# Kernel optimization log

Measured on AMD Instinct MI355X. Metric: run time of the kernel, lower is better.

The kernel has to match this reference:

```python
import jax, jax.numpy as jnp
import numpy as np

VOCAB = 32000
HIDDEN = 512
B, T = 8, 512
LN_EPS = 1e-5


def setup_inputs() -> dict:
    key = jax.random.key(0)
    ks = jax.random.split(key, 9)
    s = 0.02
    return {
        "input_ids": jax.random.randint(ks[0], (B, T), 0, VOCAB),
        "emb": jax.random.normal(ks[1], (VOCAB, HIDDEN), jnp.float32) * s,
        "w_ih": jax.random.normal(ks[2], (3 * HIDDEN, HIDDEN), jnp.float32) * s,
        "w_hh": jax.random.normal(ks[3], (3 * HIDDEN, HIDDEN), jnp.float32) * s,
        "b_ih": jnp.zeros((3 * HIDDEN,), jnp.float32),
        "b_hh": jnp.zeros((3 * HIDDEN,), jnp.float32),
        "ln_gamma": jnp.ones((HIDDEN,), jnp.float32),
        "ln_beta": jnp.zeros((HIDDEN,), jnp.float32),
        "head_w": jax.random.normal(ks[4], (VOCAB, HIDDEN), jnp.float32) * s,
        "head_b": jnp.zeros((VOCAB,), jnp.float32),
    }


def _gru_scan(xg, w_hh, b_hh):
    # xg: [T, B, 3H]  (input-side gate pre-activations, PyTorch gate order r,z,n)
    H = xg.shape[-1] // 3
    h0 = jnp.zeros((xg.shape[1], H), xg.dtype)

    def step(h, xg_t):
        hg = h @ w_hh.T + b_hh              # [B, 3H]
        xr, xz, xn = jnp.split(xg_t, 3, axis=-1)
        hr, hz, hn = jnp.split(hg, 3, axis=-1)
        r = jax.nn.sigmoid(xr + hr)
        z = jax.nn.sigmoid(xz + hz)
        n = jnp.tanh(xn + r * hn)
        h_new = (1.0 - z) * n + z * h
        return h_new, h_new

    _, hs = jax.lax.scan(step, h0, xg)
    return hs  # [T, B, H]


def reference(input_ids, emb, w_ih, w_hh, b_ih, b_hh, ln_gamma, ln_beta, head_w, head_b):
    # embedding lookup: [B, T, H]
    x = emb[input_ids]
    # precompute input-side gate pre-activations for all timesteps: [B, T, 3H]
    xg = jnp.einsum("bth,gh->btg", x, w_ih) + b_ih
    # sequential GRU over time
    hs = _gru_scan(jnp.swapaxes(xg, 0, 1), w_hh, b_hh)  # [T, B, H]
    hs = jnp.swapaxes(hs, 0, 1)                          # [B, T, H]
    # LayerNorm over hidden dim
    mu = jnp.mean(hs, axis=-1, keepdims=True)
    var = jnp.mean(jnp.square(hs - mu), axis=-1, keepdims=True)
    y = (hs - mu) * jax.lax.rsqrt(var + LN_EPS) * ln_gamma + ln_beta
    # output head: [B, T, V]
    logits = jnp.einsum("bth,vh->btv", y, head_w) + head_b
    return logits
```

## Files before the change

kernel.cpp:

```cpp
#include <hip/hip_runtime.h>
#include <hip/hip_bf16.h>
#include <stdint.h>

#define VOCAB 32000
#define HID 512
#define NB 8
#define SEQ 512
#define NG 1536
#define LN_EPS 1e-5f
#define GRU_WGS 32
#define GRU_SPIN_BUDGET (1 << 20)

typedef short bf16x8 __attribute__((ext_vector_type(8)));
typedef float f32x4 __attribute__((ext_vector_type(4)));

__device__ __forceinline__ unsigned short f2bf(float f) {
  union { float f; uint32_t u; } c; c.f = f;
  return (unsigned short)((c.u + 0x7fffu + ((c.u >> 16) & 1u)) >> 16);
}

__global__ void init_ws_kernel(unsigned short* h_state, int* flags) {
  int i = blockIdx.x * 256 + threadIdx.x;
  if (i < 2 * 16 * HID) h_state[i] = 0;
  if (i < GRU_WGS * 16) flags[i] = 0;
}

__global__ void conv_bf16_kernel(const float* __restrict__ in,
                                 unsigned short* __restrict__ out, int n4) {
  int i = blockIdx.x * 256 + threadIdx.x;
  if (i >= n4) return;
  const float4 v = ((const float4*)in)[i];
  ushort4 o;
  o.x = f2bf(v.x); o.y = f2bf(v.y); o.z = f2bf(v.z); o.w = f2bf(v.w);
  ((ushort4*)out)[i] = o;
}

__global__ void embed_kernel(const int* __restrict__ ids,
                             const float* __restrict__ emb,
                             unsigned short* __restrict__ out) {
  int row = blockIdx.x;
  int id = ids[row];
  int c = threadIdx.x * 2;
  const float2 v = *(const float2*)(emb + (size_t)id * HID + c);
  ushort2 o; o.x = f2bf(v.x); o.y = f2bf(v.y);
  *(ushort2*)(out + (size_t)row * HID + c) = o;
}

#define BM 128
#define BN 128
#define BK 32

__global__ __launch_bounds__(256, 2) void gemm_bt_kernel(
    const unsigned short* __restrict__ A, const unsigned short* __restrict__ B,
    const float* __restrict__ bias, float* __restrict__ C, int N, int nbn) {
  __shared__ unsigned short a_lds[BM * BK];
  __shared__ unsigned short b_lds[BN * BK];
  const int nwg = gridDim.x;
  const int chunk = nwg >> 3;
  const int bid = blockIdx.x;
  const int sw = (bid & 7) * chunk + (bid >> 3);
  const int bm = sw / nbn, bn = sw % nbn;
  const int tid = threadIdx.x;
  const int lane = tid & 63, wid = tid >> 6;
  const int wm = wid >> 1, wn = wid & 1;

  f32x4 acc[4][4] = {};

  for (int kt = 0; kt < HID / BK; ++kt) {
    __syncthreads();
#pragma unroll
    for (int p = 0; p < 2; ++p) {
      const int flat = (p * 256 + tid) * 16;
      const int row = flat >> 6;
      const int kb = flat & 63;
      const char* ga =
          (const char*)(A + ((size_t)(bm * BM + row) * HID + kt * BK)) + kb;
      const char* gb =
          (const char*)(B + ((size_t)(bn * BN + row) * HID + kt * BK)) + kb;
      char* la = (char*)a_lds + (size_t)(p * 256 + wid * 64) * 16;
      char* lb = (char*)b_lds + (size_t)(p * 256 + wid * 64) * 16;
      __builtin_amdgcn_global_load_lds(
          (const __attribute__((address_space(1))) void*)ga,
          (__attribute__((address_space(3))) void*)la, 16, 0, 0);
      __builtin_amdgcn_global_load_lds(
          (const __attribute__((address_space(1))) void*)gb,
          (__attribute__((address_space(3))) void*)lb, 16, 0, 0);
    }
    __syncthreads();
    bf16x8 af[4], bfr[4];
#pragma unroll
    for (int i = 0; i < 4; ++i) {
      af[i] = *(const bf16x8*)(a_lds + (wm * 64 + i * 16 + (lane & 15)) * BK +
                               (lane >> 4) * 8);
      bfr[i] = *(const bf16x8*)(b_lds + (wn * 64 + i * 16 + (lane & 15)) * BK +
                                (lane >> 4) * 8);
    }
#pragma unroll
    for (int i = 0; i < 4; ++i)
#pragma unroll
      for (int j = 0; j < 4; ++j)
        acc[i][j] =
            __builtin_amdgcn_mfma_f32_16x16x32_bf16(af[i], bfr[j], acc[i][j], 0, 0, 0);
  }
#pragma unroll
  for (int i = 0; i < 4; ++i) {
    const int mrow = bm * BM + wm * 64 + i * 16 + (lane >> 4) * 4;
#pragma unroll
    for (int j = 0; j < 4; ++j) {
      const int col = bn * BN + wn * 64 + j * 16 + (lane & 15);
      const float bv = bias[col];
#pragma unroll
      for (int r = 0; r < 4; ++r)
        C[(size_t)(mrow + r) * N + col] = acc[i][j][r] + bv;
    }
  }
}

__global__ __launch_bounds__(192, 1) void gru_kernel(
    const float* __restrict__ xg, const float* __restrict__ w_hh,
    const float* __restrict__ b_hh, float* __restrict__ hs,
    unsigned short* h_state, int* flags) {
  const int wid = blockIdx.x;
  const int tid = threadIdx.x;
  const int lane = tid & 63;
  const int g = tid >> 6;

  __shared__ float hg_lds[3 * 128];
  __shared__ float bhh_lds[48];

  bf16x8 wf[16];
  {
    const int row = g * HID + wid * 16 + (lane & 15);
    const float* wr = w_hh + (size_t)row * HID + (lane >> 4) * 8;
#pragma unroll
    for (int kk = 0; kk < 16; ++kk) {
      float4 f0 = *(const float4*)(wr + kk * 32);
      float4 f1 = *(const float4*)(wr + kk * 32 + 4);
      bf16x8 v;
      v[0] = (short)f2bf(f0.x); v[1] = (short)f2bf(f0.y);
      v[2] = (short)f2bf(f0.z); v[3] = (short)f2bf(f0.w);
      v[4] = (short)f2bf(f1.x); v[5] = (short)f2bf(f1.y);
      v[6] = (short)f2bf(f1.z); v[7] = (short)f2bf(f1.w);
      wf[kk] = v;
    }
  }
  if (tid < 48) bhh_lds[tid] = b_hh[(tid >> 4) * HID + wid * 16 + (tid & 15)];
  __syncthreads();

  const int abase = (lane & 15) * HID + (lane >> 4) * 8;
  const bool realrow = (lane & 15) < 8;
  const int myflag = (lane & 31) * 16;
  const int b8 = tid >> 4, n16 = tid & 15;
  const size_t xoff0 = (size_t)b8 * SEQ * NG + wid * 16 + n16;

  float xr = 0.f, xz = 0.f, xn = 0.f;
  if (tid < 128) {
    xr = xg[xoff0];
    xz = xg[xoff0 + HID];
    xn = xg[xoff0 + 2 * HID];
  }
  float hprev = 0.f;
  int budget = GRU_SPIN_BUDGET;

  for (int t = 0; t < SEQ; ++t) {
    const unsigned short* rd = h_state + (size_t)(t & 1) * (16 * HID);
    unsigned short* wr_ = h_state + (size_t)((t + 1) & 1) * (16 * HID);

    uint64_t hb[32];
#pragma unroll
    for (int kk = 0; kk < 32; ++kk) hb[kk] = 0;
    if (realrow) {
#pragma unroll
      for (int kk = 0; kk < 16; ++kk) {
        const uint64_t* ap = (const uint64_t*)(rd + abase + kk * 32);
        hb[2 * kk] =
            __hip_atomic_load(ap, __ATOMIC_RELAXED, __HIP_MEMORY_SCOPE_AGENT);
        hb[2 * kk + 1] = __hip_atomic_load(ap + 1, __ATOMIC_RELAXED,
                                           __HIP_MEMORY_SCOPE_AGENT);
      }
    }
    f32x4 acc = {0.f, 0.f, 0.f, 0.f};
#pragma unroll
    for (int kk = 0; kk < 16; ++kk) {
      union { uint64_t u[2]; bf16x8 v; } cv;
      cv.u[0] = hb[2 * kk]; cv.u[1] = hb[2 * kk + 1];
      acc = __builtin_amdgcn_mfma_f32_16x16x32_bf16(cv.v, wf[kk], acc, 0, 0, 0);
    }
    if (lane < 32) {
      const int m0 = (lane >> 4) * 4;
#pragma unroll
      for (int r = 0; r < 4; ++r)
        hg_lds[g * 128 + (m0 + r) * 16 + (lane & 15)] = acc[r];
    }
    __syncthreads();
    if (tid < 128) {
      const float hrv = hg_lds[tid] + bhh_lds[n16];
      const float hzv = hg_lds[128 + tid] + bhh_lds[16 + n16];
      const float hnv = hg_lds[256 + tid] + bhh_lds[32 + n16];
      const float r = 1.f / (1.f + __expf(-(xr + hrv)));
      const float z = 1.f / (1.f + __expf(-(xz + hzv)));
      const float a = xn + r * hnv;
      const float e2 = __expf(-2.f * fabsf(a));
      const float nn = copysignf((1.f - e2) / (1.f + e2), a);
      const float hnew = (1.f - z) * nn + z * hprev;
      hprev = hnew;
      hs[((size_t)b8 * SEQ + t) * HID + wid * 16 + n16] = hnew;
      const float hnb = __shfl_down(hnew, 1);
      if ((n16 & 1) == 0) {
        union { unsigned short s[2]; uint32_t u; } pk;
        pk.s[0] = f2bf(hnew); pk.s[1] = f2bf(hnb);
        uint32_t* dst = (uint32_t*)(wr_ + b8 * HID + wid * 16 + n16);
        __hip_atomic_store(dst, pk.u, __ATOMIC_RELAXED,
                           __HIP_MEMORY_SCOPE_AGENT);
      }
    }
    __syncthreads();
    if (tid == 0)
      __hip_atomic_store(flags + wid * 16, t + 1, __ATOMIC_RELAXED,
                         __HIP_MEMORY_SCOPE_AGENT);
    if (tid < 128 && t + 1 < SEQ) {
      const size_t xo = xoff0 + (size_t)(t + 1) * NG;
      xr = xg[xo]; xz = xg[xo + HID]; xn = xg[xo + 2 * HID];
    }
    if (tid < 64) {
      while (budget > 0) {
        int v = __hip_atomic_load(flags + myflag, __ATOMIC_RELAXED,
                                  __HIP_MEMORY_SCOPE_AGENT);
        if (__ballot(v >= t + 1) == ~0ULL) break;
        --budget;
        __builtin_amdgcn_s_sleep(1);
      }
    }
    __syncthreads();
  }
}

__global__ __launch_bounds__(256) void ln_kernel(
    const float* __restrict__ hs, const float* __restrict__ gamma,
    const float* __restrict__ beta, unsigned short* __restrict__ y) {
  const int row = blockIdx.x * 4 + (threadIdx.x >> 6);
  const int lane = threadIdx.x & 63;
  const float* x = hs + (size_t)row * HID + lane * 8;
  float v[8];
  *(float4*)v = *(const float4*)x;
  *(float4*)(v + 4) = *(const float4*)(x + 4);
  float s = 0.f, q = 0.f;
#pragma unroll
  for (int j = 0; j < 8; ++j) { s += v[j]; q += v[j] * v[j]; }
#pragma unroll
  for (int off = 32; off > 0; off >>= 1) {
    s += __shfl_xor(s, off);
    q += __shfl_xor(q, off);
  }
  const float mu = s * (1.f / 512.f);
  const float is = rsqrtf(q * (1.f / 512.f) - mu * mu + LN_EPS);
  const float* gp = gamma + lane * 8;
  const float* bp = beta + lane * 8;
  union { unsigned short o[8]; uint4 u; } pk;
#pragma unroll
  for (int j = 0; j < 8; ++j) pk.o[j] = f2bf((v[j] - mu) * is * gp[j] + bp[j]);
  *(uint4*)(y + (size_t)row * HID + lane * 8) = pk.u;
}

extern "C" void kernel_launch(void* const* d_in, const int* in_sizes, int n_in,
                              void* d_out, int out_size, void* d_ws,
                              size_t ws_size, hipStream_t stream) {
  const int* ids = (const int*)d_in[0];
  const float* emb = (const float*)d_in[1];
  const float* w_ih = (const float*)d_in[2];
  const float* w_hh = (const float*)d_in[3];
  const float* b_ih = (const float*)d_in[4];
  const float* b_hh = (const float*)d_in[5];
  const float* gamma = (const float*)d_in[6];
  const float* beta = (const float*)d_in[7];
  const float* head_w = (const float*)d_in[8];
  const float* head_b = (const float*)d_in[9];
  float* out = (float*)d_out;

  char* ws = (char*)d_ws;
  size_t off = 0;
  auto alloc = [&](size_t bytes) -> void* {
    void* p = ws + off;
    off = (off + bytes + 255) & ~(size_t)255;
    return p;
  };
  int* flags = (int*)alloc(GRU_WGS * 16 * sizeof(int));
  unsigned short* h_state = (unsigned short*)alloc(2 * 16 * HID * 2);
  unsigned short* A1 = (unsigned short*)alloc((size_t)NB * SEQ * HID * 2);
  unsigned short* wihb = (unsigned short*)alloc((size_t)NG * HID * 2);
  unsigned short* hwb = (unsigned short*)alloc((size_t)VOCAB * HID * 2);
  float* xg = (float*)alloc((size_t)NB * SEQ * NG * 4);
  float* hsb = (float*)alloc((size_t)NB * SEQ * HID * 4);
  unsigned short* yb = (unsigned short*)alloc((size_t)NB * SEQ * HID * 2);

  init_ws_kernel<<<64, 256, 0, stream>>>(h_state, flags);
  conv_bf16_kernel<<<(NG * HID / 4) / 256, 256, 0, stream>>>(w_ih, wihb,
                                                             NG * HID / 4);
  conv_bf16_kernel<<<(VOCAB * HID / 4) / 256, 256, 0, stream>>>(
      head_w, hwb, VOCAB * HID / 4);
  embed_kernel<<<NB * SEQ, 256, 0, stream>>>(ids, emb, A1);
  gemm_bt_kernel<<<(NB * SEQ / BM) * (NG / BN), 256, 0, stream>>>(
      A1, wihb, b_ih, xg, NG, NG / BN);
  gru_kernel<<<GRU_WGS, 192, 0, stream>>>(xg, w_hh, b_hh, hsb, h_state, flags);
  ln_kernel<<<NB * SEQ / 4, 256, 0, stream>>>(hsb, gamma, beta, yb);
  gemm_bt_kernel<<<(NB * SEQ / BM) * (VOCAB / BN), 256, 0, stream>>>(
      yb, hwb, head_b, out, VOCAB, VOCAB / BN);
}
```

Before: 1.980 ms.

## Replace GRU flag barrier with parity bits embedded in published hidden state

Drops the separate per-workgroup flag array and spin-wait barrier in the persistent GRU kernel. The low mantissa bit of every other bf16 hidden value now carries a step-parity tag, and consumers re-poll only the stale 64-bit chunks until every tag matches. This removes one store, one barrier and a flag round trip per timestep. It costs one bit of hidden-state precision and relies on the ordering of the relaxed atomic stores. The MFMA chain is also split into two accumulators for more instruction-level parallelism.

New measurement: 2.418 ms. 22.2% more time.

```diff
diff --git a/kernel.cpp b/kernel.cpp
--- a/kernel.cpp
+++ b/kernel.cpp
@@ -19,10 +19,10 @@
   return (unsigned short)((c.u + 0x7fffu + ((c.u >> 16) & 1u)) >> 16);
 }
 
-__global__ void init_ws_kernel(unsigned short* h_state, int* flags) {
+__global__ void init_ws_kernel(unsigned short* h_state) {
   int i = blockIdx.x * 256 + threadIdx.x;
-  if (i < 2 * 16 * HID) h_state[i] = 0;
-  if (i < GRU_WGS * 16) flags[i] = 0;
+  if (i < 16 * HID) h_state[i] = 0;
+  else if (i < 2 * 16 * HID) h_state[i] = 1;
 }
 
 __global__ void conv_bf16_kernel(const float* __restrict__ in,
@@ -119,7 +119,7 @@
 __global__ __launch_bounds__(192, 1) void gru_kernel(
     const float* __restrict__ xg, const float* __restrict__ w_hh,
     const float* __restrict__ b_hh, float* __restrict__ hs,
-    unsigned short* h_state, int* flags) {
+    unsigned short* h_state) {
   const int wid = blockIdx.x;
   const int tid = threadIdx.x;
   const int lane = tid & 63;
@@ -149,7 +149,6 @@
 
   const int abase = (lane & 15) * HID + (lane >> 4) * 8;
   const bool realrow = (lane & 15) < 8;
-  const int myflag = (lane & 31) * 16;
   const int b8 = tid >> 4, n16 = tid & 15;
   const size_t xoff0 = (size_t)b8 * SEQ * NG + wid * 16 + n16;
 
@@ -164,28 +163,44 @@
 
   for (int t = 0; t < SEQ; ++t) {
     const unsigned short* rd = h_state + (size_t)(t & 1) * (16 * HID);
-    unsigned short* wr_ = h_state + (size_t)((t + 1) & 1) * (16 * HID);
+    unsigned short* wpub = h_state + (size_t)((t + 1) & 1) * (16 * HID);
+    const uint32_t texp = (uint32_t)((t >> 1) & 1);
+    const uint32_t tpub = (uint32_t)(((t + 1) >> 1) & 1);
 
     uint64_t hb[32];
 #pragma unroll
     for (int kk = 0; kk < 32; ++kk) hb[kk] = 0;
-    if (realrow) {
+    uint32_t stale = realrow ? 0xFFFFFFFFu : 0u;
+    while (stale) {
 #pragma unroll
       for (int kk = 0; kk < 16; ++kk) {
         const uint64_t* ap = (const uint64_t*)(rd + abase + kk * 32);
-        hb[2 * kk] =
-            __hip_atomic_load(ap, __ATOMIC_RELAXED, __HIP_MEMORY_SCOPE_AGENT);
-        hb[2 * kk + 1] = __hip_atomic_load(ap + 1, __ATOMIC_RELAXED,
-                                           __HIP_MEMORY_SCOPE_AGENT);
+        if (stale & (1u << (2 * kk)))
+          hb[2 * kk] = __hip_atomic_load(ap, __ATOMIC_RELAXED,
+                                         __HIP_MEMORY_SCOPE_AGENT);
+        if (stale & (1u << (2 * kk + 1)))
+          hb[2 * kk + 1] = __hip_atomic_load(ap + 1, __ATOMIC_RELAXED,
+                                             __HIP_MEMORY_SCOPE_AGENT);
       }
-    }
-    f32x4 acc = {0.f, 0.f, 0.f, 0.f};
-#pragma unroll
-    for (int kk = 0; kk < 16; ++kk) {
-      union { uint64_t u[2]; bf16x8 v; } cv;
-      cv.u[0] = hb[2 * kk]; cv.u[1] = hb[2 * kk + 1];
-      acc = __builtin_amdgcn_mfma_f32_16x16x32_bf16(cv.v, wf[kk], acc, 0, 0, 0);
-    }
+#pragma unroll
+      for (int kk = 0; kk < 32; ++kk) {
+        const uint32_t lo = (uint32_t)hb[kk];
+        const uint32_t hi = (uint32_t)(hb[kk] >> 32);
+        if ((((lo ^ texp) | (hi ^ texp)) & 1u) == 0u) stale &= ~(1u << kk);
+      }
+      if (--budget <= 0) break;
+    }
+
+    f32x4 acc0 = {0.f, 0.f, 0.f, 0.f}, acc1 = {0.f, 0.f, 0.f, 0.f};
+#pragma unroll
+    for (int kk = 0; kk < 16; kk += 2) {
+      union { uint64_t u[2]; bf16x8 v; } c0, c1;
+      c0.u[0] = hb[2 * kk];     c0.u[1] = hb[2 * kk + 1];
+      c1.u[0] = hb[2 * kk + 2]; c1.u[1] = hb[2 * kk + 3];
+      acc0 = __builtin_amdgcn_mfma_f32_16x16x32_bf16(c0.v, wf[kk], acc0, 0, 0, 0);
+      acc1 = __builtin_amdgcn_mfma_f32_16x16x32_bf16(c1.v, wf[kk + 1], acc1, 0, 0, 0);
+    }
+    const f32x4 acc = acc0 + acc1;
     if (lane < 32) {
       const int m0 = (lane >> 4) * 4;
 #pragma unroll
@@ -208,28 +223,16 @@
       const float hnb = __shfl_down(hnew, 1);
       if ((n16 & 1) == 0) {
         union { unsigned short s[2]; uint32_t u; } pk;
-        pk.s[0] = f2bf(hnew); pk.s[1] = f2bf(hnb);
-        uint32_t* dst = (uint32_t*)(wr_ + b8 * HID + wid * 16 + n16);
+        pk.s[0] = (unsigned short)((f2bf(hnew) & ~(unsigned short)1) | tpub);
+        pk.s[1] = f2bf(hnb);
+        uint32_t* dst = (uint32_t*)(wpub + b8 * HID + wid * 16 + n16);
         __hip_atomic_store(dst, pk.u, __ATOMIC_RELAXED,
                            __HIP_MEMORY_SCOPE_AGENT);
       }
     }
-    __syncthreads();
-    if (tid == 0)
-      __hip_atomic_store(flags + wid * 16, t + 1, __ATOMIC_RELAXED,
-                         __HIP_MEMORY_SCOPE_AGENT);
     if (tid < 128 && t + 1 < SEQ) {
       const size_t xo = xoff0 + (size_t)(t + 1) * NG;
       xr = xg[xo]; xz = xg[xo + HID]; xn = xg[xo + 2 * HID];
-    }
-    if (tid < 64) {
-      while (budget > 0) {
-        int v = __hip_atomic_load(flags + myflag, __ATOMIC_RELAXED,
-                                  __HIP_MEMORY_SCOPE_AGENT);
-        if (__ballot(v >= t + 1) == ~0ULL) break;
-        --budget;
-        __builtin_amdgcn_s_sleep(1);
-      }
     }
     __syncthreads();
   }
@@ -284,7 +287,6 @@
     off = (off + bytes + 255) & ~(size_t)255;
     return p;
   };
-  int* flags = (int*)alloc(GRU_WGS * 16 * sizeof(int));
   unsigned short* h_state = (unsigned short*)alloc(2 * 16 * HID * 2);
   unsigned short* A1 = (unsigned short*)alloc((size_t)NB * SEQ * HID * 2);
   unsigned short* wihb = (unsigned short*)alloc((size_t)NG * HID * 2);
@@ -293,7 +295,7 @@
   float* hsb = (float*)alloc((size_t)NB * SEQ * HID * 4);
   unsigned short* yb = (unsigned short*)alloc((size_t)NB * SEQ * HID * 2);
 
-  init_ws_kernel<<<64, 256, 0, stream>>>(h_state, flags);
+  init_ws_kernel<<<64, 256, 0, stream>>>(h_state);
   conv_bf16_kernel<<<(NG * HID / 4) / 256, 256, 0, stream>>>(w_ih, wihb,
                                                              NG * HID / 4);
   conv_bf16_kernel<<<(VOCAB * HID / 4) / 256, 256, 0, stream>>>(
@@ -301,7 +303,7 @@
   embed_kernel<<<NB * SEQ, 256, 0, stream>>>(ids, emb, A1);
   gemm_bt_kernel<<<(NB * SEQ / BM) * (NG / BN), 256, 0, stream>>>(
       A1, wihb, b_ih, xg, NG, NG / BN);
-  gru_kernel<<<GRU_WGS, 192, 0, stream>>>(xg, w_hh, b_hh, hsb, h_state, flags);
+  gru_kernel<<<GRU_WGS, 192, 0, stream>>>(xg, w_hh, b_hh, hsb, h_state);
   ln_kernel<<<NB * SEQ / 4, 256, 0, stream>>>(hsb, gamma, beta, yb);
   gemm_bt_kernel<<<(NB * SEQ / BM) * (VOCAB / BN), 256, 0, stream>>>(
       yb, hwb, head_b, out, VOCAB, VOCAB / BN);
```

## Collapse GRU workgroup to a single wave to remove intra-block barriers

Applied to the files above, without the earlier changes.

Each GRU workgroup now runs one 64-lane wave that holds all three gate weight slices in registers and issues three MFMA chains per step, so the LDS exchange and the __syncthreads barriers inside each timestep are gone. Gate math is computed directly from the MFMA accumulator layout, and new hidden values are repacked through a small LDS buffer for the bf16 publish. The wait on other workgroups' flags moves to the start of each step. This shortens the per-step critical path of the sequential recurrence, at the cost of more register pressure (48 bf16x8 weight fragments) and three times the serial MFMA work in one wave.

Result: faster. 1.724 ms (-12.9%).

```diff
diff --git a/kernel.cpp b/kernel.cpp
--- a/kernel.cpp
+++ b/kernel.cpp
@@ -116,22 +116,22 @@
   }
 }
 
-__global__ __launch_bounds__(192, 1) void gru_kernel(
+__global__ __launch_bounds__(64, 1) void gru_kernel(
     const float* __restrict__ xg, const float* __restrict__ w_hh,
     const float* __restrict__ b_hh, float* __restrict__ hs,
     unsigned short* h_state, int* flags) {
   const int wid = blockIdx.x;
-  const int tid = threadIdx.x;
-  const int lane = tid & 63;
-  const int g = tid >> 6;
-
-  __shared__ float hg_lds[3 * 128];
-  __shared__ float bhh_lds[48];
-
-  bf16x8 wf[16];
-  {
-    const int row = g * HID + wid * 16 + (lane & 15);
-    const float* wr = w_hh + (size_t)row * HID + (lane >> 4) * 8;
+  const int lane = threadIdx.x;
+  const int col16 = lane & 15;
+  const int kq = lane >> 4;
+
+  __shared__ float h_pub[8][16];
+
+  bf16x8 wf[3][16];
+#pragma unroll
+  for (int g = 0; g < 3; ++g) {
+    const float* wr =
+        w_hh + (size_t)(g * HID + wid * 16 + col16) * HID + kq * 8;
 #pragma unroll
     for (int kk = 0; kk < 16; ++kk) {
       float4 f0 = *(const float4*)(wr + kk * 32);
@@ -141,30 +141,46 @@
       v[2] = (short)f2bf(f0.z); v[3] = (short)f2bf(f0.w);
       v[4] = (short)f2bf(f1.x); v[5] = (short)f2bf(f1.y);
       v[6] = (short)f2bf(f1.z); v[7] = (short)f2bf(f1.w);
-      wf[kk] = v;
-    }
-  }
-  if (tid < 48) bhh_lds[tid] = b_hh[(tid >> 4) * HID + wid * 16 + (tid & 15)];
-  __syncthreads();
-
-  const int abase = (lane & 15) * HID + (lane >> 4) * 8;
-  const bool realrow = (lane & 15) < 8;
-  const int myflag = (lane & 31) * 16;
-  const int b8 = tid >> 4, n16 = tid & 15;
-  const size_t xoff0 = (size_t)b8 * SEQ * NG + wid * 16 + n16;
-
-  float xr = 0.f, xz = 0.f, xn = 0.f;
-  if (tid < 128) {
-    xr = xg[xoff0];
-    xz = xg[xoff0 + HID];
-    xn = xg[xoff0 + 2 * HID];
-  }
-  float hprev = 0.f;
+      wf[g][kk] = v;
+    }
+  }
+  const float bh_r = b_hh[0 * HID + wid * 16 + col16];
+  const float bh_z = b_hh[1 * HID + wid * 16 + col16];
+  const float bh_n = b_hh[2 * HID + wid * 16 + col16];
+
+  const int abase = col16 * HID + kq * 8;
+  const bool realrow = col16 < 8;
+  const bool owner = lane < 32;
+  const int bbase = kq * 4;
+
+  float xr[4], xz[4], xn[4];
+#pragma unroll
+  for (int r = 0; r < 4; ++r) { xr[r] = 0.f; xz[r] = 0.f; xn[r] = 0.f; }
+  if (owner) {
+#pragma unroll
+    for (int r = 0; r < 4; ++r) {
+      const size_t xo = (size_t)(bbase + r) * SEQ * NG + wid * 16 + col16;
+      xr[r] = xg[xo];
+      xz[r] = xg[xo + HID];
+      xn[r] = xg[xo + 2 * HID];
+    }
+  }
+  float hprev[4] = {0.f, 0.f, 0.f, 0.f};
   int budget = GRU_SPIN_BUDGET;
 
   for (int t = 0; t < SEQ; ++t) {
+    while (budget > 0) {
+      int v = t;
+      if (lane < 32)
+        v = __hip_atomic_load(flags + lane * 16, __ATOMIC_RELAXED,
+                              __HIP_MEMORY_SCOPE_AGENT);
+      if (__ballot(v >= t) == ~0ULL) break;
+      --budget;
+      __builtin_amdgcn_s_sleep(1);
+    }
+
     const unsigned short* rd = h_state + (size_t)(t & 1) * (16 * HID);
-    unsigned short* wr_ = h_state + (size_t)((t + 1) & 1) * (16 * HID);
+    unsigned short* wpub = h_state + (size_t)((t + 1) & 1) * (16 * HID);
 
     uint64_t hb[32];
 #pragma unroll
@@ -179,59 +195,64 @@
                                            __HIP_MEMORY_SCOPE_AGENT);
       }
     }
-    f32x4 acc = {0.f, 0.f, 0.f, 0.f};
+
+    f32x4 ar = {0.f, 0.f, 0.f, 0.f};
+    f32x4 az = {0.f, 0.f, 0.f, 0.f};
+    f32x4 an = {0.f, 0.f, 0.f, 0.f};
 #pragma unroll
     for (int kk = 0; kk < 16; ++kk) {
       union { uint64_t u[2]; bf16x8 v; } cv;
       cv.u[0] = hb[2 * kk]; cv.u[1] = hb[2 * kk + 1];
-      acc = __builtin_amdgcn_mfma_f32_16x16x32_bf16(cv.v, wf[kk], acc, 0, 0, 0);
-    }
-    if (lane < 32) {
-      const int m0 = (lane >> 4) * 4;
-#pragma unroll
-      for (int r = 0; r < 4; ++r)
-        hg_lds[g * 128 + (m0 + r) * 16 + (lane & 15)] = acc[r];
-    }
-    __syncthreads();
-    if (tid < 128) {
-      const float hrv = hg_lds[tid] + bhh_lds[n16];
-      const float hzv = hg_lds[128 + tid] + bhh_lds[16 + n16];
-      const float hnv = hg_lds[256 + tid] + bhh_lds[32 + n16];
-      const float r = 1.f / (1.f + __expf(-(xr + hrv)));
-      const float z = 1.f / (1.f + __expf(-(xz + hzv)));
-      const float a = xn + r * hnv;
-      const float e2 = __expf(-2.f * fabsf(a));
-      const float nn = copysignf((1.f - e2) / (1.f + e2), a);
-      const float hnew = (1.f - z) * nn + z * hprev;
-      hprev = hnew;
-      hs[((size_t)b8 * SEQ + t) * HID + wid * 16 + n16] = hnew;
-      const float hnb = __shfl_down(hnew, 1);
-      if ((n16 & 1) == 0) {
-        union { unsigned short s[2]; uint32_t u; } pk;
-        pk.s[0] = f2bf(hnew); pk.s[1] = f2bf(hnb);
-        uint32_t* dst = (uint32_t*)(wr_ + b8 * HID + wid * 16 + n16);
-        __hip_atomic_store(dst, pk.u, __ATOMIC_RELAXED,
-                           __HIP_MEMORY_SCOPE_AGENT);
+      ar = __builtin_amdgcn_mfma_f32_16x16x32_bf16(cv.v, wf[0][kk], ar, 0, 0, 0);
+      az = __builtin_amdgcn_mfma_f32_16x16x32_bf16(cv.v, wf[1][kk], az, 0, 0, 0);
+      an = __builtin_amdgcn_mfma_f32_16x16x32_bf16(cv.v, wf[2][kk], an, 0, 0, 0);
+    }
+
+    float hnew[4];
+    if (owner) {
+#pragma unroll
+      for (int r = 0; r < 4; ++r) {
+        const float rg = 1.f / (1.f + __expf(-(xr[r] + ar[r] + bh_r)));
+        const float zg = 1.f / (1.f + __expf(-(xz[r] + az[r] + bh_z)));
+        const float a = xn[r] + rg * (an[r] + bh_n);
+        const float e2 = __expf(-2.f * fabsf(a));
+        const float nn = copysignf((1.f - e2) / (1.f + e2), a);
+        hnew[r] = (1.f - zg) * nn + zg * hprev[r];
+        hprev[r] = hnew[r];
+        h_pub[bbase + r][col16] = hnew[r];
       }
     }
-    __syncthreads();
-    if (tid == 0)
+    asm volatile("" ::: "memory");
+    {
+      const int tb = lane >> 3;
+      const int tc = (lane & 7) * 2;
+      const float2 hp = *(const float2*)&h_pub[tb][tc];
+      union { unsigned short s[2]; uint32_t u; } pk;
+      pk.s[0] = f2bf(hp.x);
+      pk.s[1] = f2bf(hp.y);
+      uint32_t* dst = (uint32_t*)(wpub + tb * HID + wid * 16 + tc);
+      __hip_atomic_store(dst, pk.u, __ATOMIC_RELAXED,
+                         __HIP_MEMORY_SCOPE_AGENT);
+    }
+    asm volatile("s_waitcnt vmcnt(0)" ::: "memory");
+    if (lane == 0)
       __hip_atomic_store(flags + wid * 16, t + 1, __ATOMIC_RELAXED,
                          __HIP_MEMORY_SCOPE_AGENT);
-    if (tid < 128 && t + 1 < SEQ) {
-      const size_t xo = xoff0 + (size_t)(t + 1) * NG;
-      xr = xg[xo]; xz = xg[xo + HID]; xn = xg[xo + 2 * HID];
-    }
-    if (tid < 64) {
-      while (budget > 0) {
-        int v = __hip_atomic_load(flags + myflag, __ATOMIC_RELAXED,
-                                  __HIP_MEMORY_SCOPE_AGENT);
-        if (__ballot(v >= t + 1) == ~0ULL) break;
-        --budget;
-        __builtin_amdgcn_s_sleep(1);
+    if (owner) {
+#pragma unroll
+      for (int r = 0; r < 4; ++r)
+        hs[((size_t)(bbase + r) * SEQ + t) * HID + wid * 16 + col16] = hnew[r];
+      if (t + 1 < SEQ) {
+#pragma unroll
+        for (int r = 0; r < 4; ++r) {
+          const size_t xo = (size_t)(bbase + r) * SEQ * NG +
+                            (size_t)(t + 1) * NG + wid * 16 + col16;
+          xr[r] = xg[xo];
+          xz[r] = xg[xo + HID];
+          xn[r] = xg[xo + 2 * HID];
+        }
       }
     }
-    __syncthreads();
   }
 }
 
@@ -301,7 +322,7 @@
   embed_kernel<<<NB * SEQ, 256, 0, stream>>>(ids, emb, A1);
   gemm_bt_kernel<<<(NB * SEQ / BM) * (NG / BN), 256, 0, stream>>>(
       A1, wihb, b_ih, xg, NG, NG / BN);
-  gru_kernel<<<GRU_WGS, 192, 0, stream>>>(xg, w_hh, b_hh, hsb, h_state, flags);
+  gru_kernel<<<GRU_WGS, 64, 0, stream>>>(xg, w_hh, b_hh, hsb, h_state, flags);
   ln_kernel<<<NB * SEQ / 4, 256, 0, stream>>>(hsb, gamma, beta, yb);
   gemm_bt_kernel<<<(NB * SEQ / BM) * (VOCAB / BN), 256, 0, stream>>>(
       yb, hwb, head_b, out, VOCAB, VOCAB / BN);
```
